# Optimization experiments

Measured on AMD Instinct MI355X. Metric: run time of the kernel, lower is better.

## Reference

```python
import jax, jax.numpy as jnp
import numpy as np

N_NODES = 20000
N_EDGES = 160000
F_IN = 128
H1 = 1024  # 128 * out_channels
H2 = 512   # 64 * out_channels
OUT = 8    # out_channels


def graph_conv(x, src, dst, w_rel, b_rel, w_root):
    # PyG GraphConv(aggr='mean'): out = lin_rel(mean_{j->i} x_j) + lin_root(x_i)
    n = x.shape[0]
    agg = jax.ops.segment_sum(x[src], dst, num_segments=n)          # [N, F_in]
    deg = jax.ops.segment_sum(jnp.ones((src.shape[0],), x.dtype), dst, num_segments=n)
    mean = agg / jnp.maximum(deg, 1.0)[:, None]
    return mean @ w_rel + b_rel + x @ w_root


def setup_inputs() -> dict:
    key = jax.random.key(0)
    ks = jax.random.split(key, 12)
    x = jax.random.normal(ks[0], (N_NODES, F_IN), dtype=jnp.float32)
    edge_index = jax.random.randint(ks[1], (2, N_EDGES), 0, N_NODES, dtype=jnp.int64)

    def lin(k, fi, fo):
        return jax.random.normal(k, (fi, fo), dtype=jnp.float32) / np.sqrt(fi)

    return {
        "x": x,
        "edge_index": edge_index,
        "w1_rel": lin(ks[2], F_IN, H1), "b1": jnp.zeros((H1,), jnp.float32), "w1_root": lin(ks[3], F_IN, H1),
        "w2_rel": lin(ks[4], H1, H2), "b2": jnp.zeros((H2,), jnp.float32), "w2_root": lin(ks[5], H1, H2),
        "wmu_rel": lin(ks[6], H2, OUT), "bmu": jnp.zeros((OUT,), jnp.float32), "wmu_root": lin(ks[7], H2, OUT),
        "wls_rel": lin(ks[8], H2, OUT), "bls": jnp.zeros((OUT,), jnp.float32), "wls_root": lin(ks[9], H2, OUT),
    }


def reference(x, edge_index, w1_rel, b1, w1_root, w2_rel, b2, w2_root,
              wmu_rel, bmu, wmu_root, wls_rel, bls, wls_root):
    src, dst = edge_index[0], edge_index[1]
    h = jax.nn.relu(graph_conv(x, src, dst, w1_rel, b1, w1_root))
    h = jax.nn.relu(graph_conv(h, src, dst, w2_rel, b2, w2_root))
    mu = graph_conv(h, src, dst, wmu_rel, bmu, wmu_root)
    logstd = graph_conv(h, src, dst, wls_rel, bls, wls_root)
    return (mu, logstd)
```

## Files before the change

kernel.cpp:

```cpp
#include <hip/hip_runtime.h>

typedef __attribute__((ext_vector_type(8))) short short8;
typedef __attribute__((ext_vector_type(4))) float f32x4;
typedef unsigned long long u64;

__device__ __forceinline__ unsigned short f2bf(float f) {
  union { float f; unsigned u; } v; v.f = f;
  unsigned u = v.u;
  unsigned r = (u + 0x7FFFu + ((u >> 16) & 1u)) >> 16;
  return (unsigned short)r;
}
__device__ __forceinline__ float bf2f(unsigned short s) {
  union { unsigned u; float f; } v; v.u = ((unsigned)s) << 16;
  return v.f;
}

__device__ __forceinline__ void gl_lds16(const unsigned short* g, unsigned short* l) {
  __builtin_amdgcn_global_load_lds(
      (const __attribute__((address_space(1))) void*)g,
      (__attribute__((address_space(3))) void*)l, 16, 0, 0);
}


__global__ void init_kernel(int* a, int n, int* b, int nb, int* flag,
                            const long long* edges, int nslots, int n_nodes) {
  int i = blockIdx.x * blockDim.x + threadIdx.x;
  int stride = gridDim.x * blockDim.x;
  for (int j = i; j < n; j += stride) a[j] = 0;
  for (int j = i; j < nb; j += stride) b[j] = 0;
  if (i == 0) *flag = 1;
  for (int j = i; j < nslots; j += stride) {
    long long v = edges[j];
    if (v < 0 || v >= n_nodes) atomicAnd(flag, 0);
  }
}

__device__ __forceinline__ int edge_at(const void* p, int is64, size_t idx) {
  return is64 ? (int)((const long long*)p)[idx] : ((const int*)p)[idx];
}

__global__ void count_kernel(const void* edges, int E, const int* flag, int* deg) {
  int is64 = *flag;
  int i = blockIdx.x * blockDim.x + threadIdx.x;
  int stride = gridDim.x * blockDim.x;
  for (int e = i; e < E; e += stride) {
    int d = edge_at(edges, is64, (size_t)E + e);
    atomicAdd(&deg[d], 1);
  }
}

__global__ void scan_kernel(const int* __restrict__ deg, int* __restrict__ rs,
                            float* __restrict__ invdeg, int n) {
  __shared__ int ssum[1024];
  int tid = threadIdx.x;
  int chunk = (n + 1023) >> 10;
  int start = tid * chunk;
  int end = min(start + chunk, n);
  int s = 0;
  for (int i = start; i < end; ++i) s += deg[i];
  ssum[tid] = s;
  __syncthreads();
  for (int off = 1; off < 1024; off <<= 1) {
    int t = (tid >= off) ? ssum[tid - off] : 0;
    __syncthreads();
    ssum[tid] += t;
    __syncthreads();
  }
  int run = (tid ? ssum[tid - 1] : 0);
  if (tid == 0) rs[0] = 0;
  for (int i = start; i < end; ++i) {
    int d = deg[i];
    run += d;
    rs[i + 1] = run;
    invdeg[i] = 1.0f / fmaxf((float)d, 1.0f);
  }
}

__global__ void fill_kernel(const void* edges, int E, const int* flag,
                            const int* __restrict__ rs, int* cursor, int* col_src) {
  int is64 = *flag;
  int i = blockIdx.x * blockDim.x + threadIdx.x;
  int stride = gridDim.x * blockDim.x;
  for (int e = i; e < E; e += stride) {
    int d = edge_at(edges, is64, (size_t)E + e);
    int s = edge_at(edges, is64, (size_t)e);
    int p = atomicAdd(&cursor[d], 1);
    col_src[rs[d] + p] = s;
  }
}


__global__ void agg1_kernel(const float* __restrict__ x,
                            const int* __restrict__ rs, const int* __restrict__ cs,
                            const float* __restrict__ invdeg,
                            unsigned short* __restrict__ A1) {
  int node = blockIdx.x;
  int f = threadIdx.x;
  float xi = x[(size_t)node * 128 + f];
  float acc = 0.f;
  int e1 = rs[node + 1];
  for (int e = rs[node]; e < e1; ++e) {
    acc += x[(size_t)cs[e] * 128 + f];
  }
  A1[(size_t)node * 256 + f] = f2bf(acc * invdeg[node]);
  A1[(size_t)node * 256 + 128 + f] = f2bf(xi);
}

__global__ void agg2_kernel(const unsigned short* __restrict__ P2,
                            const int* __restrict__ rs, const int* __restrict__ cs,
                            const float* __restrict__ invdeg,
                            const float* __restrict__ b2,
                            unsigned short* __restrict__ h2) {
  int node = blockIdx.x;
  int f0 = threadIdx.x * 4;
  float acc0 = 0.f, acc1 = 0.f, acc2 = 0.f, acc3 = 0.f;
  int e1 = rs[node + 1];
  for (int e = rs[node]; e < e1; ++e) {
    int s = cs[e];
    u64 w = *reinterpret_cast<const u64*>(P2 + (size_t)s * 1024 + f0);
    acc0 += bf2f((unsigned short)w);
    acc1 += bf2f((unsigned short)(w >> 16));
    acc2 += bf2f((unsigned short)(w >> 32));
    acc3 += bf2f((unsigned short)(w >> 48));
  }
  float inv = invdeg[node];
  u64 wr = *reinterpret_cast<const u64*>(P2 + (size_t)node * 1024 + 512 + f0);
  float v0 = fmaxf(acc0 * inv + bf2f((unsigned short)wr) + b2[f0 + 0], 0.f);
  float v1 = fmaxf(acc1 * inv + bf2f((unsigned short)(wr >> 16)) + b2[f0 + 1], 0.f);
  float v2 = fmaxf(acc2 * inv + bf2f((unsigned short)(wr >> 32)) + b2[f0 + 2], 0.f);
  float v3 = fmaxf(acc3 * inv + bf2f((unsigned short)(wr >> 48)) + b2[f0 + 3], 0.f);
  u64 o = (u64)f2bf(v0) | ((u64)f2bf(v1) << 16) | ((u64)f2bf(v2) << 32) | ((u64)f2bf(v3) << 48);
  *reinterpret_cast<u64*>(h2 + (size_t)node * 512 + f0) = o;
}

__global__ void head_agg_kernel(const float* __restrict__ P3,
                                const int* __restrict__ rs, const int* __restrict__ cs,
                                const float* __restrict__ invdeg,
                                const float* __restrict__ bmu, const float* __restrict__ bls,
                                float* __restrict__ outmu, float* __restrict__ outls, int M) {
  int idx = blockIdx.x * blockDim.x + threadIdx.x;
  int node = idx >> 4;
  int c = idx & 15;
  if (node >= M) return;
  int relc = (c < 8) ? c : (16 + (c - 8));
  float acc = 0.f;
  int e1 = rs[node + 1];
  for (int e = rs[node]; e < e1; ++e) acc += P3[(size_t)cs[e] * 128 + relc];
  float v = acc * invdeg[node] + P3[(size_t)node * 128 + relc + 8]
          + ((c < 8) ? bmu[c] : bls[c - 8]);
  if (c < 8) outmu[(size_t)node * 8 + c] = v;
  else outls[(size_t)node * 8 + (c - 8)] = v;
}


__device__ __forceinline__ void ttile(const float* __restrict__ src, int Nw,
                                      unsigned short* __restrict__ dst, int ldd,
                                      int rowoff, int coloff,
                                      int tileIdx, int tilesN, float (*tile)[33]) {
  int tk = tileIdx / tilesN, tn = tileIdx % tilesN;
  int k0 = tk * 32, n0 = tn * 32;
  int tx = threadIdx.x & 31, ty = threadIdx.x >> 5;
#pragma unroll
  for (int s = 0; s < 4; ++s)
    tile[ty + s * 8][tx] = src[(size_t)(k0 + ty + s * 8) * Nw + n0 + tx];
  __syncthreads();
#pragma unroll
  for (int s = 0; s < 4; ++s)
    dst[(size_t)(rowoff + n0 + ty + s * 8) * ldd + coloff + k0 + tx] =
        f2bf(tile[tx][ty + s * 8]);
}

__global__ void wtrans_all_kernel(const float* __restrict__ w1_rel, const float* __restrict__ w1_root,
                                  const float* __restrict__ w2_rel, const float* __restrict__ w2_root,
                                  const float* __restrict__ wmu_rel, const float* __restrict__ wmu_root,
                                  const float* __restrict__ wls_rel, const float* __restrict__ wls_root,
                                  unsigned short* __restrict__ Bt1,
                                  unsigned short* __restrict__ Bt2,
                                  unsigned short* __restrict__ Bt3) {
  __shared__ float tile[32][33];
  int b = blockIdx.x;
  if (b < 128)       ttile(w1_rel, 1024, Bt1, 256, 0, 0, b, 32, tile);
  else if (b < 256)  ttile(w1_root, 1024, Bt1, 256, 0, 128, b - 128, 32, tile);
  else if (b < 768)  ttile(w2_rel, 512, Bt2, 1024, 0, 0, b - 256, 16, tile);
  else if (b < 1280) ttile(w2_root, 512, Bt2, 1024, 512, 0, b - 768, 16, tile);
  else {
    int idx = (b - 1280) * 256 + threadIdx.x;
    int n = idx >> 9, k = idx & 511;
    float v;
    if (n < 8) v = wmu_rel[(size_t)k * 8 + n];
    else if (n < 16) v = wmu_root[(size_t)k * 8 + (n - 8)];
    else if (n < 24) v = wls_rel[(size_t)k * 8 + (n - 16)];
    else v = wls_root[(size_t)k * 8 + (n - 24)];
    Bt3[(size_t)n * 512 + k] = f2bf(v);
  }
}

__launch_bounds__(256, 3)
__global__ void gemm_kernel(const unsigned short* __restrict__ A, int lda,
                            const unsigned short* __restrict__ Bt, int ldb,
                            const float* __restrict__ bias,
                            void* __restrict__ outp, int ldo,
                            int M, int N, int K, int relu, int out_f32, int gx) {
  __shared__ unsigned short As[3 * 4096];
  __shared__ unsigned short Bs[3 * 4096];
  int tid = threadIdx.x;
  int lane = tid & 63;
  int w = tid >> 6;
  int wr = w >> 1, wc = w & 1;
  int lr = lane & 15, lk = lane >> 4;

  int nwg = gridDim.x, orig = blockIdx.x;
  int q = nwg >> 3, r = nwg & 7;
  int xcd = orig & 7, lid = orig >> 3;
  int swz = (xcd < r ? xcd * (q + 1) : r * (q + 1) + (xcd - r) * q) + lid;
  int m0 = (swz / gx) * 128, n0 = (swz % gx) * 128;

  f32x4 acc[4][4];
#pragma unroll
  for (int i = 0; i < 4; ++i)
#pragma unroll
    for (int j = 0; j < 4; ++j) acc[i][j] = (f32x4)0.0f;

  int r0 = tid >> 2;
  int slog = (tid & 3) ^ ((r0 >> 1) & 3);
  const unsigned short* gA = A + (size_t)(m0 + r0) * lda + slog * 8;
  const unsigned short* gB = Bt + (size_t)(n0 + r0) * ldb + slog * 8;
  size_t a64 = (size_t)64 * lda, b64 = (size_t)64 * ldb;
  unsigned short* wa = As + w * 512;
  unsigned short* wb = Bs + w * 512;

  int sw8 = (lk ^ ((lr >> 1) & 3)) * 8;

  int nt = K >> 5;
  gl_lds16(gA, wa); gl_lds16(gA + a64, wa + 2048);
  gl_lds16(gB, wb); gl_lds16(gB + b64, wb + 2048);
  gA += 32; gB += 32;
  gl_lds16(gA, wa + 4096); gl_lds16(gA + a64, wa + 6144);
  gl_lds16(gB, wb + 4096); gl_lds16(gB + b64, wb + 6144);
  gA += 32; gB += 32;
  asm volatile("s_waitcnt vmcnt(4)" ::: "memory");
  __builtin_amdgcn_s_barrier();

  int bufR = 0, bufS = 2;
  for (int t = 0; t < nt; ++t) {
    if (t + 2 < nt) {
      unsigned short* sa = As + bufS * 4096 + w * 512;
      unsigned short* sb = Bs + bufS * 4096 + w * 512;
      gl_lds16(gA, sa); gl_lds16(gA + a64, sa + 2048);
      gl_lds16(gB, sb); gl_lds16(gB + b64, sb + 2048);
      gA += 32; gB += 32;
    }
    const unsigned short* as_ = As + bufR * 4096;
    const unsigned short* bs_ = Bs + bufR * 4096;
    short8 af[4], bfr[4];
#pragma unroll
    for (int i = 0; i < 4; ++i) {
      af[i]  = *reinterpret_cast<const short8*>(&as_[(wr * 64 + i * 16 + lr) * 32 + sw8]);
      bfr[i] = *reinterpret_cast<const short8*>(&bs_[(wc * 64 + i * 16 + lr) * 32 + sw8]);
    }
    __builtin_amdgcn_s_setprio(1);
#pragma unroll
    for (int i = 0; i < 4; ++i)
#pragma unroll
      for (int j = 0; j < 4; ++j)
        acc[i][j] = __builtin_amdgcn_mfma_f32_16x16x32_bf16(af[i], bfr[j], acc[i][j], 0, 0, 0);
    __builtin_amdgcn_s_setprio(0);
    if (t + 1 < nt) {
      if (t + 2 < nt)
        asm volatile("s_waitcnt vmcnt(4) lgkmcnt(0)" ::: "memory");
      else
        asm volatile("s_waitcnt vmcnt(0) lgkmcnt(0)" ::: "memory");
      __builtin_amdgcn_s_barrier();
    }
    bufR = (bufR == 2) ? 0 : bufR + 1;
    bufS = (bufS == 2) ? 0 : bufS + 1;
  }

#pragma unroll
  for (int i = 0; i < 4; ++i) {
    int row_b = m0 + wr * 64 + i * 16 + lk * 4;
#pragma unroll
    for (int j = 0; j < 4; ++j) {
      int col = n0 + wc * 64 + j * 16 + lr;
      float bv = bias ? bias[col] : 0.f;
#pragma unroll
      for (int rr = 0; rr < 4; ++rr) {
        int row = row_b + rr;
        if (row < M) {
          float v = acc[i][j][rr] + bv;
          if (relu) v = fmaxf(v, 0.f);
          if (out_f32) ((float*)outp)[(size_t)row * ldo + col] = v;
          else ((unsigned short*)outp)[(size_t)row * ldo + col] = f2bf(v);
        }
      }
    }
  }
}


extern "C" void kernel_launch(void* const* d_in, const int* in_sizes, int n_in,
                              void* d_out, int out_size, void* d_ws, size_t ws_size,
                              hipStream_t stream) {
  const float* x = (const float*)d_in[0];
  const void* edge = d_in[1];
  const float* w1_rel = (const float*)d_in[2];
  const float* b1 = (const float*)d_in[3];
  const float* w1_root = (const float*)d_in[4];
  const float* w2_rel = (const float*)d_in[5];
  const float* b2 = (const float*)d_in[6];
  const float* w2_root = (const float*)d_in[7];
  const float* wmu_rel = (const float*)d_in[8];
  const float* bmu = (const float*)d_in[9];
  const float* wmu_root = (const float*)d_in[10];
  const float* wls_rel = (const float*)d_in[11];
  const float* bls = (const float*)d_in[12];
  const float* wls_root = (const float*)d_in[13];

  const int FIN = 128, H1 = 1024, H2 = 512;
  const int M = in_sizes[0] / FIN;
  const int E = in_sizes[1] / 2;
  const int Mpad = ((M + 127) / 128) * 128;
  const int gy = Mpad / 128;

  char* ws = (char*)d_ws;
  size_t off = 0;
  auto alloc = [&](size_t bytes) -> char* {
    char* p = ws + off;
    off = (off + bytes + 255) & ~(size_t)255;
    return p;
  };
  int* flag = (int*)alloc(4);
  int* deg = (int*)alloc((size_t)M * 4);
  int* cursor = (int*)alloc((size_t)M * 4);
  int* rs = (int*)alloc((size_t)(M + 1) * 4);
  float* invdeg = (float*)alloc((size_t)M * 4);
  int* cs = (int*)alloc((size_t)E * 4);
  unsigned short* A1 = (unsigned short*)alloc((size_t)Mpad * 256 * 2);
  unsigned short* h1 = (unsigned short*)alloc((size_t)Mpad * 1024 * 2);
  unsigned short* P2 = (unsigned short*)alloc((size_t)Mpad * 1024 * 2);
  unsigned short* h2 = (unsigned short*)alloc((size_t)Mpad * 512 * 2);
  float* P3 = (float*)alloc((size_t)Mpad * 128 * 4);
  unsigned short* Bt1 = (unsigned short*)alloc((size_t)H1 * 256 * 2);
  unsigned short* Bt2 = (unsigned short*)alloc((size_t)1024 * 1024 * 2);
  unsigned short* Bt3 = (unsigned short*)alloc((size_t)128 * 512 * 2);

  init_kernel<<<64, 256, 0, stream>>>(deg, M, cursor, M, flag, (const long long*)edge, 2048, M);
  count_kernel<<<256, 256, 0, stream>>>(edge, E, flag, deg);
  scan_kernel<<<1, 1024, 0, stream>>>(deg, rs, invdeg, M);
  fill_kernel<<<256, 256, 0, stream>>>(edge, E, flag, rs, cursor, cs);

  wtrans_all_kernel<<<1344, 256, 0, stream>>>(w1_rel, w1_root, w2_rel, w2_root,
                                              wmu_rel, wmu_root, wls_rel, wls_root,
                                              Bt1, Bt2, Bt3);

  agg1_kernel<<<M, 128, 0, stream>>>(x, rs, cs, invdeg, A1);
  gemm_kernel<<<(H1 / 128) * gy, 256, 0, stream>>>(
      A1, 256, Bt1, 256, b1, h1, 1024, M, H1, 256, 1, 0, H1 / 128);

  gemm_kernel<<<(1024 / 128) * gy, 256, 0, stream>>>(
      h1, 1024, Bt2, 1024, nullptr, P2, 1024, M, 1024, 1024, 0, 0, 1024 / 128);
  agg2_kernel<<<M, 128, 0, stream>>>(P2, rs, cs, invdeg, b2, h2);

  gemm_kernel<<<1 * gy, 256, 0, stream>>>(
      h2, 512, Bt3, 512, nullptr, P3, 128, M, 128, 512, 0, 1, 1);
  float* outmu = (float*)d_out;
  float* outls = outmu + (size_t)M * 8;
  head_agg_kernel<<<(M * 16 + 255) / 256, 256, 0, stream>>>(
      P3, rs, cs, invdeg, bmu, bls, outmu, outls, M);
}
```

Measured before the change: 278.0 us.

## Add 256x256-tile 8-wave GEMM with phased LDS pipeline for large layers

Adds a new GEMM kernel with 256x256 output tiles, 512 threads, a 128 KB LDS double buffer split into k-halves, and an eight-phase schedule. Each phase interleaves global-to-LDS loads with MFMA work and uses s_setprio around the MFMAs. It replaces the 128x128 kernel for the two large layer GEMMs, which raises data reuse per tile and cuts global traffic. The trade-off is fewer workgroups (about 316 for 20000 rows), more padded rows, and high register and LDS pressure, so occupancy may suffer.

New measurement: 323.6 us. +16.4%, slower.

```diff
diff --git a/kernel.cpp b/kernel.cpp
--- a/kernel.cpp
+++ b/kernel.cpp
@@ -195,12 +195,130 @@
   }
 }
 
+#define R_(d, mat, kh) ((((d) * 2 + (mat)) * 2 + (kh)) * 8192)
+
+__launch_bounds__(512, 2)
+__global__ void gemm256_kernel(const unsigned short* __restrict__ A, int lda,
+                               const unsigned short* __restrict__ Bt, int ldb,
+                               const float* __restrict__ bias,
+                               void* __restrict__ outp, int ldo,
+                               int M, int N, int K, int relu, int out_f32, int gx) {
+  __shared__ unsigned short sh[65536];
+  const int tid = threadIdx.x;
+  const int lane = tid & 63;
+  const int w = tid >> 6;
+  const int wr = w >> 2, wc = w & 3;
+  const int lr = lane & 15, lk = lane >> 4;
+  const int lk8 = lk * 8;
+  const int wrb = (wr * 128 + lr) * 32;
+  const int wcb = (wc * 64 + lr) * 32;
+
+  int nwg = gridDim.x, orig = blockIdx.x;
+  int q = nwg >> 3, r = nwg & 7;
+  int xcd = orig & 7, lid = orig >> 3;
+  int swz = (xcd < r ? xcd * (q + 1) : r * (q + 1) + (xcd - r) * q) + lid;
+  int m0 = (swz / gx) * 256, n0 = (swz % gx) * 256;
+
+  f32x4 acc[8][4];
+#pragma unroll
+  for (int i = 0; i < 8; ++i)
+#pragma unroll
+    for (int j = 0; j < 4; ++j) acc[i][j] = (f32x4)0.0f;
+
+  const int r4 = tid >> 2, s4 = tid & 3;
+  const unsigned short* pA = A + (size_t)(m0 + r4) * lda + s4 * 8;
+  const unsigned short* pB = Bt + (size_t)(n0 + r4) * ldb + s4 * 8;
+
+  auto STG = [&](int d, int mat, int kh, int kt) {
+    const unsigned short* g = (mat ? pB : pA) + (size_t)kt * 64 + kh * 32;
+    size_t ld = mat ? (size_t)ldb : (size_t)lda;
+    unsigned short* lb = sh + R_(d, mat, kh) + w * 512;
+    gl_lds16(g, lb);
+    gl_lds16(g + 128 * ld, lb + 4096);
+  };
+
+  STG(0, 0, 0, 0); STG(0, 0, 1, 0); STG(0, 1, 0, 0); STG(0, 1, 1, 0);
+  STG(1, 0, 0, 1); STG(1, 0, 1, 1); STG(1, 1, 0, 1); STG(1, 1, 1, 1);
+  asm volatile("s_waitcnt vmcnt(8)" ::: "memory");
+  __builtin_amdgcn_s_barrier();
+
+#define DSB(dd, kk)                                                            \
+  _Pragma("unroll") for (int nf = 0; nf < 4; ++nf)                             \
+      bfr[nf] = *reinterpret_cast<const short8*>(                              \
+          &sh[R_(dd, 1, kk) + wcb + nf * 512 + lk8]);
+
+#define PH(dd, kk, mh, DOB, STGSTMT, ENDW)                                     \
+  {                                                                            \
+    if (DOB) { DSB(dd, kk) }                                                   \
+    short8 af[4];                                                              \
+    _Pragma("unroll") for (int mf = 0; mf < 4; ++mf)                           \
+        af[mf] = *reinterpret_cast<const short8*>(                             \
+            &sh[R_(dd, 0, kk) + wrb + mh * 2048 + mf * 512 + lk8]);            \
+    STGSTMT;                                                                   \
+    __builtin_amdgcn_s_barrier();                                              \
+    asm volatile("s_waitcnt lgkmcnt(0)" ::: "memory");                         \
+    __builtin_amdgcn_s_setprio(1);                                             \
+    _Pragma("unroll") for (int mf = 0; mf < 4; ++mf)                           \
+        _Pragma("unroll") for (int nf = 0; nf < 4; ++nf)                       \
+            acc[mh * 4 + mf][nf] = __builtin_amdgcn_mfma_f32_16x16x32_bf16(    \
+                af[mf], bfr[nf], acc[mh * 4 + mf][nf], 0, 0, 0);               \
+    __builtin_amdgcn_s_setprio(0);                                             \
+    ENDW;                                                                      \
+    __builtin_amdgcn_s_barrier();                                              \
+  }
+
+  const int niter = K >> 7;
+  short8 bfr[4];
+  for (int i = 0; i < niter; ++i) {
+    const bool first = (i == 0), last = (i == niter - 1);
+    const int t1 = 2 * i + 1, t2 = 2 * i + 2, t3 = 2 * i + 3;
+
+    PH(0, 0, 0, 1, if (!first) { STG(1, 0, 1, t1); }, )
+    PH(0, 0, 1, 0, if (!first) { STG(1, 1, 1, t1); },
+       if (last) { asm volatile("s_waitcnt vmcnt(4)" ::: "memory"); }
+       else      { asm volatile("s_waitcnt vmcnt(6)" ::: "memory"); })
+    PH(0, 1, 0, 1, if (!last) { STG(0, 0, 0, t2); }, )
+    PH(0, 1, 1, 0, if (!last) { STG(0, 1, 0, t2); },
+       if (last) { asm volatile("s_waitcnt vmcnt(2)" ::: "memory"); }
+       else      { asm volatile("s_waitcnt vmcnt(6)" ::: "memory"); })
+    PH(1, 0, 0, 1, if (!last) { STG(0, 0, 1, t2); }, )
+    PH(1, 0, 1, 0, if (!last) { STG(0, 1, 1, t2); },
+       if (last) { asm volatile("s_waitcnt vmcnt(0)" ::: "memory"); }
+       else      { asm volatile("s_waitcnt vmcnt(6)" ::: "memory"); })
+    PH(1, 1, 0, 1, if (!last) { STG(1, 0, 0, t3); }, )
+    PH(1, 1, 1, 0, if (!last) { STG(1, 1, 0, t3); },
+       if (!last) { asm volatile("s_waitcnt vmcnt(6)" ::: "memory"); })
+  }
+#undef PH
+#undef DSB
+
+#pragma unroll
+  for (int mf8 = 0; mf8 < 8; ++mf8) {
+    int row_b = m0 + wr * 128 + mf8 * 16 + lk * 4;
+#pragma unroll
+    for (int nf = 0; nf < 4; ++nf) {
+      int col = n0 + wc * 64 + nf * 16 + lr;
+      float bv = bias ? bias[col] : 0.f;
+#pragma unroll
+      for (int rr = 0; rr < 4; ++rr) {
+        int row = row_b + rr;
+        if (row < M) {
+          float v = acc[mf8][nf][rr] + bv;
+          if (relu) v = fmaxf(v, 0.f);
+          if (out_f32) ((float*)outp)[(size_t)row * ldo + col] = v;
+          else ((unsigned short*)outp)[(size_t)row * ldo + col] = f2bf(v);
+        }
+      }
+    }
+  }
+}
+
 __launch_bounds__(256, 3)
-__global__ void gemm_kernel(const unsigned short* __restrict__ A, int lda,
-                            const unsigned short* __restrict__ Bt, int ldb,
-                            const float* __restrict__ bias,
-                            void* __restrict__ outp, int ldo,
-                            int M, int N, int K, int relu, int out_f32, int gx) {
+__global__ void gemm128_kernel(const unsigned short* __restrict__ A, int lda,
+                               const unsigned short* __restrict__ Bt, int ldb,
+                               const float* __restrict__ bias,
+                               void* __restrict__ outp, int ldo,
+                               int M, int N, int K, int relu, int out_f32, int gx) {
   __shared__ unsigned short As[3 * 4096];
   __shared__ unsigned short Bs[3 * 4096];
   int tid = threadIdx.x;
@@ -228,7 +346,6 @@
   size_t a64 = (size_t)64 * lda, b64 = (size_t)64 * ldb;
   unsigned short* wa = As + w * 512;
   unsigned short* wb = Bs + w * 512;
-
   int sw8 = (lk ^ ((lr >> 1) & 3)) * 8;
 
   int nt = K >> 5;
@@ -319,8 +436,9 @@
   const int FIN = 128, H1 = 1024, H2 = 512;
   const int M = in_sizes[0] / FIN;
   const int E = in_sizes[1] / 2;
-  const int Mpad = ((M + 127) / 128) * 128;
-  const int gy = Mpad / 128;
+  const int Mpad = ((M + 255) / 256) * 256;
+  const int gy256 = Mpad / 256;
+  const int gy128 = Mpad / 128;
 
   char* ws = (char*)d_ws;
   size_t off = 0;
@@ -354,14 +472,14 @@
                                               Bt1, Bt2, Bt3);
 
   agg1_kernel<<<M, 128, 0, stream>>>(x, rs, cs, invdeg, A1);
-  gemm_kernel<<<(H1 / 128) * gy, 256, 0, stream>>>(
-      A1, 256, Bt1, 256, b1, h1, 1024, M, H1, 256, 1, 0, H1 / 128);
-
-  gemm_kernel<<<(1024 / 128) * gy, 256, 0, stream>>>(
-      h1, 1024, Bt2, 1024, nullptr, P2, 1024, M, 1024, 1024, 0, 0, 1024 / 128);
+  gemm256_kernel<<<(H1 / 256) * gy256, 512, 0, stream>>>(
+      A1, 256, Bt1, 256, b1, h1, 1024, M, H1, 256, 1, 0, H1 / 256);
+
+  gemm256_kernel<<<(1024 / 256) * gy256, 512, 0, stream>>>(
+      h1, 1024, Bt2, 1024, nullptr, P2, 1024, M, 1024, 1024, 0, 0, 1024 / 256);
   agg2_kernel<<<M, 128, 0, stream>>>(P2, rs, cs, invdeg, b2, h2);
 
-  gemm_kernel<<<1 * gy, 256, 0, stream>>>(
+  gemm128_kernel<<<1 * gy128, 256, 0, stream>>>(
       h2, 512, Bt3, 512, nullptr, P3, 128, M, 128, 512, 0, 1, 1);
   float* outmu = (float*)d_out;
   float* outls = outmu + (size_t)M * 8;
```

## Add 128x256-tile GEMM with 8 waves for the two large layers

Applied to the files above, without the earlier changes.

Adds a GEMM kernel with 512 threads that computes 128x256 output tiles, so each A tile loaded into LDS is reused across twice as many columns. The first two dense layers now use this kernel and the original 128x128 kernel is kept only for the small head GEMM. The intent is to cut global and LDS traffic for A and the per-block overhead. In exchange the grid has half as many blocks and each block uses more LDS, which may reduce occupancy or leave CUs idle on the tail wave.

New measurement: 284.1 us. 2.2% more time.

```diff
diff --git a/kernel.cpp b/kernel.cpp
--- a/kernel.cpp
+++ b/kernel.cpp
@@ -195,12 +195,111 @@
   }
 }
 
+__launch_bounds__(512, 4)
+__global__ void gemm_wide_kernel(const unsigned short* __restrict__ A, int lda,
+                                 const unsigned short* __restrict__ Bt, int ldb,
+                                 const float* __restrict__ bias,
+                                 void* __restrict__ outp, int ldo,
+                                 int M, int N, int K, int relu, int out_f32, int gx) {
+  __shared__ unsigned short As[3 * 4096];
+  __shared__ unsigned short Bs[3 * 8192];
+  const int tid = threadIdx.x;
+  const int lane = tid & 63;
+  const int w = tid >> 6;
+  const int wr = w >> 2, wc = w & 3;
+  const int lr = lane & 15, lk = lane >> 4;
+  const int sw8 = (lk ^ ((lr >> 1) & 3)) * 8;
+
+  int nwg = gridDim.x, orig = blockIdx.x;
+  int q = nwg >> 3, r = nwg & 7;
+  int xcd = orig & 7, lid = orig >> 3;
+  int swz = (xcd < r ? xcd * (q + 1) : r * (q + 1) + (xcd - r) * q) + lid;
+  int m0 = (swz / gx) * 128, n0 = (swz % gx) * 256;
+
+  f32x4 acc[4][4];
+#pragma unroll
+  for (int i = 0; i < 4; ++i)
+#pragma unroll
+    for (int j = 0; j < 4; ++j) acc[i][j] = (f32x4)0.0f;
+
+  const int r0 = tid >> 2;
+  const int slog = ((tid & 3) ^ ((r0 >> 1) & 3)) * 8;
+  const unsigned short* gA = A + (size_t)(m0 + r0) * lda + slog;
+  const unsigned short* gB = Bt + (size_t)(n0 + r0) * ldb + slog;
+  size_t b128 = (size_t)128 * ldb;
+  unsigned short* wa = As + w * 512;
+  unsigned short* wb = Bs + w * 512;
+
+  auto STG = [&](int s, int t) {
+    const unsigned short* a = gA + (size_t)t * 32;
+    const unsigned short* b = gB + (size_t)t * 32;
+    gl_lds16(a, wa + s * 4096);
+    gl_lds16(b, wb + s * 8192);
+    gl_lds16(b + b128, wb + s * 8192 + 4096);
+  };
+
+  int nt = K >> 5;
+  STG(0, 0);
+  STG(1, 1);
+  asm volatile("s_waitcnt vmcnt(3)" ::: "memory");
+  __builtin_amdgcn_s_barrier();
+
+  int bufR = 0, bufS = 2;
+  for (int t = 0; t < nt; ++t) {
+    if (t + 2 < nt) STG(bufS, t + 2);
+    const unsigned short* as_ = As + bufR * 4096;
+    const unsigned short* bs_ = Bs + bufR * 8192;
+    short8 af[4], bf[4];
+#pragma unroll
+    for (int i = 0; i < 4; ++i) {
+      af[i] = *reinterpret_cast<const short8*>(&as_[(wr * 64 + i * 16 + lr) * 32 + sw8]);
+      bf[i] = *reinterpret_cast<const short8*>(&bs_[(wc * 64 + i * 16 + lr) * 32 + sw8]);
+    }
+    __builtin_amdgcn_s_setprio(1);
+#pragma unroll
+    for (int i = 0; i < 4; ++i)
+#pragma unroll
+      for (int j = 0; j < 4; ++j)
+        acc[i][j] = __builtin_amdgcn_mfma_f32_16x16x32_bf16(af[i], bf[j], acc[i][j], 0, 0, 0);
+    __builtin_amdgcn_s_setprio(0);
+    if (t + 1 < nt) {
+      if (t + 2 < nt)
+        asm volatile("s_waitcnt vmcnt(3) lgkmcnt(0)" ::: "memory");
+      else
+        asm volatile("s_waitcnt vmcnt(0) lgkmcnt(0)" ::: "memory");
+      __builtin_amdgcn_s_barrier();
+    }
+    bufR = (bufR == 2) ? 0 : bufR + 1;
+    bufS = (bufS == 2) ? 0 : bufS + 1;
+  }
+
+#pragma unroll
+  for (int i = 0; i < 4; ++i) {
+    int row_b = m0 + wr * 64 + i * 16 + lk * 4;
+#pragma unroll
+    for (int j = 0; j < 4; ++j) {
+      int col = n0 + wc * 64 + j * 16 + lr;
+      float bv = bias ? bias[col] : 0.f;
+#pragma unroll
+      for (int rr = 0; rr < 4; ++rr) {
+        int row = row_b + rr;
+        if (row < M) {
+          float v = acc[i][j][rr] + bv;
+          if (relu) v = fmaxf(v, 0.f);
+          if (out_f32) ((float*)outp)[(size_t)row * ldo + col] = v;
+          else ((unsigned short*)outp)[(size_t)row * ldo + col] = f2bf(v);
+        }
+      }
+    }
+  }
+}
+
 __launch_bounds__(256, 3)
-__global__ void gemm_kernel(const unsigned short* __restrict__ A, int lda,
-                            const unsigned short* __restrict__ Bt, int ldb,
-                            const float* __restrict__ bias,
-                            void* __restrict__ outp, int ldo,
-                            int M, int N, int K, int relu, int out_f32, int gx) {
+__global__ void gemm128_kernel(const unsigned short* __restrict__ A, int lda,
+                               const unsigned short* __restrict__ Bt, int ldb,
+                               const float* __restrict__ bias,
+                               void* __restrict__ outp, int ldo,
+                               int M, int N, int K, int relu, int out_f32, int gx) {
   __shared__ unsigned short As[3 * 4096];
   __shared__ unsigned short Bs[3 * 4096];
   int tid = threadIdx.x;
@@ -228,7 +327,6 @@
   size_t a64 = (size_t)64 * lda, b64 = (size_t)64 * ldb;
   unsigned short* wa = As + w * 512;
   unsigned short* wb = Bs + w * 512;
-
   int sw8 = (lk ^ ((lr >> 1) & 3)) * 8;
 
   int nt = K >> 5;
@@ -354,14 +452,14 @@
                                               Bt1, Bt2, Bt3);
 
   agg1_kernel<<<M, 128, 0, stream>>>(x, rs, cs, invdeg, A1);
-  gemm_kernel<<<(H1 / 128) * gy, 256, 0, stream>>>(
-      A1, 256, Bt1, 256, b1, h1, 1024, M, H1, 256, 1, 0, H1 / 128);
-
-  gemm_kernel<<<(1024 / 128) * gy, 256, 0, stream>>>(
-      h1, 1024, Bt2, 1024, nullptr, P2, 1024, M, 1024, 1024, 0, 0, 1024 / 128);
+  gemm_wide_kernel<<<(H1 / 256) * gy, 512, 0, stream>>>(
+      A1, 256, Bt1, 256, b1, h1, 1024, M, H1, 256, 1, 0, H1 / 256);
+
+  gemm_wide_kernel<<<(1024 / 256) * gy, 512, 0, stream>>>(
+      h1, 1024, Bt2, 1024, nullptr, P2, 1024, M, 1024, 1024, 0, 0, 1024 / 256);
   agg2_kernel<<<M, 128, 0, stream>>>(P2, rs, cs, invdeg, b2, h2);
 
-  gemm_kernel<<<1 * gy, 256, 0, stream>>>(
+  gemm128_kernel<<<1 * gy, 256, 0, stream>>>(
       h2, 512, Bt3, 512, nullptr, P3, 128, M, 128, 512, 0, 1, 1);
   float* outmu = (float*)d_out;
   float* outls = outmu + (size_t)M * 8;
```
